# Optimization experiments

Hardware: AMD Instinct MI355X
Metric: run time of the kernel (lower is better)

## Reference

```python
import jax, jax.numpy as jnp
import numpy as np

HEADS = 12
HEAD_DIM = 64  # dim=768 // heads=12
NEG = -1e9


def setup_inputs() -> dict:
    key = jax.random.key(0)
    k1, k2, k3 = jax.random.split(key, 3)
    dim = HEADS * HEAD_DIM
    x = jax.random.normal(k1, (8, 1024, dim), dtype=jnp.float32)
    W_qkv = jax.random.normal(k2, (dim, 3 * dim), dtype=jnp.float32) * (dim ** -0.5)
    b_qkv = jnp.zeros((3 * dim,), dtype=jnp.float32)
    W_out = jax.random.normal(k3, (dim, dim), dtype=jnp.float32) * (dim ** -0.5)
    b_out = jnp.zeros((dim,), dtype=jnp.float32)
    return {"x": x, "W_qkv": W_qkv, "b_qkv": b_qkv, "W_out": W_out, "b_out": b_out}


def reference(x, W_qkv, b_qkv, W_out, b_out):
    B, T, C = x.shape
    qkv = x @ W_qkv + b_qkv                      # [B,T,3C]
    q, k, v = jnp.split(qkv, 3, axis=-1)
    # [B,T,C] -> [B,H,T,Dh]
    def split_heads(t):
        return t.reshape(B, T, HEADS, HEAD_DIM).transpose(0, 2, 1, 3)
    q, k, v = split_heads(q), split_heads(k), split_heads(v)
    att = jnp.einsum('bhqd,bhkd->bhqk', q, k) / jnp.sqrt(jnp.float32(HEAD_DIM))
    causal = jnp.tril(jnp.ones((T, T), dtype=bool))  # [T,T]
    att = jnp.where(causal[None, None], att, NEG)
    att = jax.nn.softmax(att, axis=-1)
    out = jnp.einsum('bhqk,bhkd->bhqd', att, v)  # [B,H,T,Dh]
    out = out.transpose(0, 2, 1, 3).reshape(B, T, C)
    return out @ W_out + b_out
```

## Files before the change

### kernel.cpp

```cpp
#include <hip/hip_runtime.h>
#include <hip/hip_bf16.h>

typedef unsigned short u16;
typedef unsigned int u32;
typedef __attribute__((ext_vector_type(8))) short short8;
typedef __attribute__((ext_vector_type(4))) float f32x4;
typedef __attribute__((ext_vector_type(16))) float f32x16;
typedef __attribute__((ext_vector_type(4))) unsigned int uint4v;

__device__ __forceinline__ u16 f2bf(float f) {
    union { float f; unsigned int u; } v; v.f = f;
    unsigned int u = v.u;
    return (u16)((u + 0x7FFFu + ((u >> 16) & 1u)) >> 16);
}
__device__ __forceinline__ u32 pk2(float a, float b) {
    return ((u32)f2bf(b) << 16) | (u32)f2bf(a);
}

__global__ void k_convert(const float* __restrict__ x, u16* __restrict__ o, int n4) {
    int i = blockIdx.x * blockDim.x + threadIdx.x;
    if (i < n4) {
        float4 v = ((const float4*)x)[i];
        ushort4 r;
        r.x = f2bf(v.x); r.y = f2bf(v.y); r.z = f2bf(v.z); r.w = f2bf(v.w);
        ((ushort4*)o)[i] = r;
    }
}

__global__ void k_transpose_bf(const float* __restrict__ W, u16* __restrict__ Wt, int K, int N) {
    __shared__ u16 t[32][33];
    int n0 = blockIdx.x * 32, k0 = blockIdx.y * 32;
    int tx = threadIdx.x, ty = threadIdx.y;
    #pragma unroll
    for (int i = 0; i < 4; i++) {
        t[ty + i * 8][tx] = f2bf(W[(long)(k0 + ty + i * 8) * N + n0 + tx]);
    }
    __syncthreads();
    #pragma unroll
    for (int i = 0; i < 4; i++) {
        Wt[(long)(n0 + ty + i * 8) * K + k0 + tx] = t[tx][ty + i * 8];
    }
}

__global__ void k_vt(const u16* __restrict__ qkv, u16* __restrict__ vt) {
    __shared__ u16 s[32][33];
    int t0 = blockIdx.x * 32, d0 = blockIdx.y * 32, bh = blockIdx.z;
    int b = bh / 12, h = bh - b * 12;
    int tx = threadIdx.x, ty = threadIdx.y;
    const u16* src = qkv + (size_t)(b * 1024 + t0) * 2304 + 1536 + h * 64 + d0;
    #pragma unroll
    for (int i = 0; i < 4; i++) {
        s[ty + i * 8][tx] = src[(size_t)(ty + i * 8) * 2304 + tx];
    }
    __syncthreads();
    u16* dst = vt + (size_t)bh * 65536 + (size_t)d0 * 1024 + t0;
    #pragma unroll
    for (int i = 0; i < 4; i++) {
        dst[(size_t)(ty + i * 8) * 1024 + tx] = s[tx][ty + i * 8];
    }
}

template<int EPI>
__global__ __launch_bounds__(256) void k_gemm_bt(
    const u16* __restrict__ A, const u16* __restrict__ Bt, const float* __restrict__ bias,
    float* __restrict__ Cf, u16* __restrict__ Cb,
    int M, int N, int K)
{
    __shared__ u16 lA[128][40];
    __shared__ u16 lB[128][40];
    int tid = threadIdx.x;
    int wid = tid >> 6, lane = tid & 63;
    int wm = wid >> 1, wn = wid & 1;
    int ln = lane & 15, gp = lane >> 4;
    int gm0 = blockIdx.x * 128, gn0 = blockIdx.y * 128;

    f32x4 zf = {0.f, 0.f, 0.f, 0.f};
    f32x4 acc[4][4];
    #pragma unroll
    for (int i = 0; i < 4; i++)
        #pragma unroll
        for (int j = 0; j < 4; j++) acc[i][j] = zf;

    int sr = tid >> 2;
    int sc = (tid & 3) * 8;

    for (int k0 = 0; k0 < K; k0 += 32) {
        #pragma unroll
        for (int j = 0; j < 2; j++) {
            int r = sr + j * 64;
            *(uint4v*)&lA[r][sc] = *(const uint4v*)&A[(long)(gm0 + r) * K + k0 + sc];
            *(uint4v*)&lB[r][sc] = *(const uint4v*)&Bt[(long)(gn0 + r) * K + k0 + sc];
        }
        __syncthreads();
        short8 af[4], bfr[4];
        #pragma unroll
        for (int i = 0; i < 4; i++) {
            af[i]  = *(const short8*)&lA[wm * 64 + i * 16 + ln][gp * 8];
            bfr[i] = *(const short8*)&lB[wn * 64 + i * 16 + ln][gp * 8];
        }
        #pragma unroll
        for (int i = 0; i < 4; i++)
            #pragma unroll
            for (int j = 0; j < 4; j++)
                acc[i][j] = __builtin_amdgcn_mfma_f32_16x16x32_bf16(af[i], bfr[j], acc[i][j], 0, 0, 0);
        __syncthreads();
    }

    #pragma unroll
    for (int i = 0; i < 4; i++) {
        #pragma unroll
        for (int j = 0; j < 4; j++) {
            #pragma unroll
            for (int r = 0; r < 4; r++) {
                int m = gm0 + wm * 64 + i * 16 + gp * 4 + r;
                int n = gn0 + wn * 64 + j * 16 + ln;
                float v = acc[i][j][r] + bias[n];
                if (EPI == 0) Cf[(long)m * N + n] = v;
                else          Cb[(long)m * N + n] = f2bf(v);
            }
        }
    }
}

__global__ __launch_bounds__(64, 3) void k_attn(
    const u16* __restrict__ qkv, const u16* __restrict__ Vt,
    u16* __restrict__ O)
{
    __shared__ u16 sK[2048];
    __shared__ u16 sV[2048];
    int lane = threadIdx.x;
    int l31 = lane & 31, hi = lane >> 5;
    int bx = blockIdx.x;
    int qtq = bx / 96, bh = bx - qtq * 96;
    int qt = 31 - qtq, q0 = qt * 32;
    int b = bh / 12, h = bh - b * 12;
    const u16* Qb  = qkv + (size_t)(b * 1024) * 2304 + h * 64;
    const u16* Kbb = Qb + 768;
    const u16* Vb  = Vt + (size_t)bh * 65536;

    short8 qf[4];
    #pragma unroll
    for (int ch = 0; ch < 4; ch++)
        qf[ch] = *(const short8*)&Qb[(size_t)(q0 + l31) * 2304 + ch * 16 + hi * 8];

    int rK = lane >> 3, cK = lane & 7;
    int rV = lane >> 2, cV = lane & 3;

    uint4v rk[4], rv[4];
    auto gload = [&](int kt) {
        #pragma unroll
        for (int j = 0; j < 4; j++) {
            int r = j * 8 + rK;
            rk[j] = *(const uint4v*)&Kbb[(size_t)(kt + r) * 2304 + cK * 8];
        }
        #pragma unroll
        for (int j = 0; j < 4; j++) {
            int r = j * 16 + rV;
            rv[j] = *(const uint4v*)&Vb[(size_t)r * 1024 + kt + cV * 8];
        }
    };
    auto swrite = [&]() {
        #pragma unroll
        for (int j = 0; j < 4; j++) {
            int r = j * 8 + rK;
            *(uint4v*)&sK[r * 64 + ((cK ^ (r & 7)) * 8)] = rk[j];
        }
        #pragma unroll
        for (int j = 0; j < 4; j++) {
            int r = j * 16 + rV;
            *(uint4v*)&sV[r * 32 + ((cV ^ (r & 3) ^ ((r >> 2) & 3)) * 8)] = rv[j];
        }
    };

    f32x16 o0 = {}, o1 = {};
    float mrun = -INFINITY, lsum = 0.f;
    const float SC = 0.18033688011f;
    int swl = l31 & 7;
    int swv = (l31 & 3) ^ ((l31 >> 2) & 3);

    int nit = qt + 1;
    gload(0);
    swrite();
    for (int it = 0; it < nit; it++) {
        int kt = it * 32;
        if (it + 1 < nit) gload(kt + 32);
        f32x16 sa = {}, sb = {};
        {
            short8 kf0 = *(const short8*)&sK[l31 * 64 + (((0 + hi) ^ swl) * 8)];
            short8 kf1 = *(const short8*)&sK[l31 * 64 + (((2 + hi) ^ swl) * 8)];
            short8 kf2 = *(const short8*)&sK[l31 * 64 + (((4 + hi) ^ swl) * 8)];
            short8 kf3 = *(const short8*)&sK[l31 * 64 + (((6 + hi) ^ swl) * 8)];
            sa = __builtin_amdgcn_mfma_f32_32x32x16_bf16(kf0, qf[0], sa, 0, 0, 0);
            sb = __builtin_amdgcn_mfma_f32_32x32x16_bf16(kf2, qf[2], sb, 0, 0, 0);
            sa = __builtin_amdgcn_mfma_f32_32x32x16_bf16(kf1, qf[1], sa, 0, 0, 0);
            sb = __builtin_amdgcn_mfma_f32_32x32x16_bf16(kf3, qf[3], sb, 0, 0, 0);
        }
        float raw[16];
        #pragma unroll
        for (int r = 0; r < 16; r++) raw[r] = sa[r] + sb[r];
        if (it == nit - 1) {
            #pragma unroll
            for (int r = 0; r < 16; r++) {
                int crow = (r & 3) + 8 * (r >> 2) + 4 * hi;
                raw[r] = (crow <= l31) ? raw[r] : -1e30f;
            }
        }
        float t8[8];
        #pragma unroll
        for (int i = 0; i < 8; i++) t8[i] = fmaxf(raw[i], raw[i + 8]);
        float t4a = fmaxf(t8[0], t8[1]), t4b = fmaxf(t8[2], t8[3]);
        float t4c = fmaxf(t8[4], t8[5]), t4d = fmaxf(t8[6], t8[7]);
        float tm = fmaxf(fmaxf(t4a, t4b), fmaxf(t4c, t4d));
        tm = fmaxf(tm, __shfl_xor(tm, 32));
        float stm = tm * SC;
        if (!__all(stm - mrun <= 8.0f)) {
            float mn = fmaxf(mrun, stm);
            float scale = exp2f(mrun - mn);
            lsum *= scale;
            #pragma unroll
            for (int r = 0; r < 16; r++) { o0[r] *= scale; o1[r] *= scale; }
            mrun = mn;
        }
        float ps[16];
        float rs = 0.f;
        #pragma unroll
        for (int r = 0; r < 16; r++) {
            ps[r] = exp2f(fmaf(raw[r], SC, -mrun));
            rs += ps[r];
        }
        rs += __shfl_xor(rs, 32);
        lsum += rs;
        u32 c[8], sw[8];
        #pragma unroll
        for (int i = 0; i < 8; i++) c[i] = pk2(ps[2 * i], ps[2 * i + 1]);
        #pragma unroll
        for (int i = 0; i < 8; i++) sw[i] = (u32)__shfl_xor((int)c[i], 32);
        union { u32 u[4]; short8 s8; } pb0, pb1;
        pb0.u[0] = hi ? sw[2] : c[0];
        pb0.u[1] = hi ? sw[3] : c[1];
        pb0.u[2] = hi ? c[2]  : sw[0];
        pb0.u[3] = hi ? c[3]  : sw[1];
        pb1.u[0] = hi ? sw[6] : c[4];
        pb1.u[1] = hi ? sw[7] : c[5];
        pb1.u[2] = hi ? c[6]  : sw[4];
        pb1.u[3] = hi ? c[7]  : sw[5];
        #pragma unroll
        for (int kh = 0; kh < 2; kh++) {
            const short8* pbp = kh ? &pb1.s8 : &pb0.s8;
            int p = (((kh * 2 + hi) ^ swv) * 8);
            short8 vf0 = *(const short8*)&sV[l31 * 32 + p];
            short8 vf1 = *(const short8*)&sV[(32 + l31) * 32 + p];
            o0 = __builtin_amdgcn_mfma_f32_32x32x16_bf16(vf0, *pbp, o0, 0, 0, 0);
            o1 = __builtin_amdgcn_mfma_f32_32x32x16_bf16(vf1, *pbp, o1, 0, 0, 0);
        }
        if (it + 1 < nit) swrite();
    }

    float inv = 1.0f / lsum;
    int t = q0 + l31;
    size_t base = ((size_t)(b * 1024 + t)) * 768 + h * 64;
    #pragma unroll
    for (int rq = 0; rq < 4; rq++) {
        ushort4 u0, u1;
        u0.x = f2bf(o0[4 * rq + 0] * inv); u0.y = f2bf(o0[4 * rq + 1] * inv);
        u0.z = f2bf(o0[4 * rq + 2] * inv); u0.w = f2bf(o0[4 * rq + 3] * inv);
        u1.x = f2bf(o1[4 * rq + 0] * inv); u1.y = f2bf(o1[4 * rq + 1] * inv);
        u1.z = f2bf(o1[4 * rq + 2] * inv); u1.w = f2bf(o1[4 * rq + 3] * inv);
        *(ushort4*)&O[base + rq * 8 + hi * 4]      = u0;
        *(ushort4*)&O[base + 32 + rq * 8 + hi * 4] = u1;
    }
}

extern "C" void kernel_launch(void* const* d_in, const int* in_sizes, int n_in,
                              void* d_out, int out_size, void* d_ws, size_t ws_size,
                              hipStream_t stream)
{
    const float* x     = (const float*)d_in[0];
    const float* W_qkv = (const float*)d_in[1];
    const float* b_qkv = (const float*)d_in[2];
    const float* W_out = (const float*)d_in[3];
    const float* b_out = (const float*)d_in[4];
    float* out = (float*)d_out;

    char* w = (char*)d_ws;
    u16* xb   = (u16*)w; w += (size_t)8192 * 768 * 2;
    u16* wqt  = (u16*)w; w += (size_t)2304 * 768 * 2;
    u16* wot  = (u16*)w; w += (size_t)768 * 768 * 2;
    u16* qkv  = (u16*)w; w += (size_t)8192 * 2304 * 2;
    u16* vt   = (u16*)w; w += (size_t)96 * 64 * 1024 * 2;
    u16* ao   = (u16*)w; w += (size_t)8192 * 768 * 2;

    k_convert<<<dim3(6144), 256, 0, stream>>>(x, xb, 1572864);
    k_transpose_bf<<<dim3(72, 24), dim3(32, 8), 0, stream>>>(W_qkv, wqt, 768, 2304);
    k_transpose_bf<<<dim3(24, 24), dim3(32, 8), 0, stream>>>(W_out, wot, 768, 768);
    k_gemm_bt<2><<<dim3(64, 18), 256, 0, stream>>>(xb, wqt, b_qkv, nullptr, qkv, 8192, 2304, 768);
    k_vt<<<dim3(32, 2, 96), dim3(32, 8), 0, stream>>>(qkv, vt);
    k_attn<<<dim3(3072), 64, 0, stream>>>(qkv, vt, ao);
    k_gemm_bt<0><<<dim3(64, 6), 256, 0, stream>>>(ao, wot, b_out, out, nullptr, 8192, 768, 768);
}
```

Before: 135.7 us.

## Triple-buffer GEMM tiles with direct global-to-LDS loads and swizzled layout

Rewrites the bf16 GEMM main loop to prefetch three K-slices ahead using global_load_lds, so global loads go straight into shared memory instead of passing through registers. Loads are overlapped with MFMA compute, with explicit vmcnt waits and barriers. The padded LDS layout is replaced by an XOR swizzle to avoid bank conflicts, and MFMA sections raise wave priority. This adds LDS footprint (three buffers) and relies on hand-managed waitcnt counts being correct.

```diff
diff --git a/kernel.cpp b/kernel.cpp
--- a/kernel.cpp
+++ b/kernel.cpp
@@ -8,6 +8,9 @@
 typedef __attribute__((ext_vector_type(16))) float f32x16;
 typedef __attribute__((ext_vector_type(4))) unsigned int uint4v;
 
+#define VMW(n) asm volatile("s_waitcnt vmcnt(" #n ")" ::: "memory")
+#define BARRIER() do { asm volatile("" ::: "memory"); __builtin_amdgcn_s_barrier(); asm volatile("" ::: "memory"); } while (0)
+
 __device__ __forceinline__ u16 f2bf(float f) {
     union { float f; unsigned int u; } v; v.f = f;
     unsigned int u = v.u;
@@ -15,6 +18,10 @@
 }
 __device__ __forceinline__ u32 pk2(float a, float b) {
     return ((u32)f2bf(b) << 16) | (u32)f2bf(a);
+}
+__device__ __forceinline__ void gload_lds16(const u16* g, u16* l) {
+    __builtin_amdgcn_global_load_lds((const __attribute__((address_space(1))) void*)g,
+                                     (__attribute__((address_space(3))) void*)l, 16, 0, 0);
 }
 
 __global__ void k_convert(const float* __restrict__ x, u16* __restrict__ o, int n4) {
@@ -66,8 +73,8 @@
     float* __restrict__ Cf, u16* __restrict__ Cb,
     int M, int N, int K)
 {
-    __shared__ u16 lA[128][40];
-    __shared__ u16 lB[128][40];
+    __shared__ u16 lA[3][128][32];
+    __shared__ u16 lB[3][128][32];
     int tid = threadIdx.x;
     int wid = tid >> 6, lane = tid & 63;
     int wm = wid >> 1, wn = wid & 1;
@@ -81,29 +88,57 @@
         #pragma unroll
         for (int j = 0; j < 4; j++) acc[i][j] = zf;
 
-    int sr = tid >> 2;
-    int sc = (tid & 3) * 8;
-
-    for (int k0 = 0; k0 < K; k0 += 32) {
-        #pragma unroll
-        for (int j = 0; j < 2; j++) {
-            int r = sr + j * 64;
-            *(uint4v*)&lA[r][sc] = *(const uint4v*)&A[(long)(gm0 + r) * K + k0 + sc];
-            *(uint4v*)&lB[r][sc] = *(const uint4v*)&Bt[(long)(gn0 + r) * K + k0 + sc];
-        }
-        __syncthreads();
+    int srow = wid * 32 + (lane >> 2);
+    int scol = (((lane & 3) ^ ((lane >> 3) & 3))) * 8;
+    const u16* gA0 = &A [(size_t)(gm0 + srow) * K + scol];
+    const u16* gA1 = gA0 + (size_t)16 * K;
+    const u16* gB0 = &Bt[(size_t)(gn0 + srow) * K + scol];
+    const u16* gB1 = gB0 + (size_t)16 * K;
+
+    int rc = (gp ^ ((ln >> 1) & 3)) * 8;
+
+    auto stage = [&](int k0, int bb) {
+        gload_lds16(gA0 + k0, &lA[bb][wid * 32][0]);
+        gload_lds16(gA1 + k0, &lA[bb][wid * 32 + 16][0]);
+        gload_lds16(gB0 + k0, &lB[bb][wid * 32][0]);
+        gload_lds16(gB1 + k0, &lB[bb][wid * 32 + 16][0]);
+    };
+    auto compute = [&](int bb) {
         short8 af[4], bfr[4];
         #pragma unroll
         for (int i = 0; i < 4; i++) {
-            af[i]  = *(const short8*)&lA[wm * 64 + i * 16 + ln][gp * 8];
-            bfr[i] = *(const short8*)&lB[wn * 64 + i * 16 + ln][gp * 8];
-        }
+            af[i]  = *(const short8*)&lA[bb][wm * 64 + i * 16 + ln][rc];
+            bfr[i] = *(const short8*)&lB[bb][wn * 64 + i * 16 + ln][rc];
+        }
+        __builtin_amdgcn_s_setprio(1);
         #pragma unroll
         for (int i = 0; i < 4; i++)
             #pragma unroll
             for (int j = 0; j < 4; j++)
                 acc[i][j] = __builtin_amdgcn_mfma_f32_16x16x32_bf16(af[i], bfr[j], acc[i][j], 0, 0, 0);
-        __syncthreads();
+        __builtin_amdgcn_s_setprio(0);
+    };
+
+    int nk = K >> 5;
+    stage(0, 0);
+    stage(32, 1);
+    stage(64, 2);
+    VMW(8);
+    BARRIER();
+    #pragma unroll 3
+    for (int t = 0; t < nk; ++t) {
+        int c = t % 3;
+        compute(c);
+        BARRIER();
+        if (t + 3 < nk) {
+            stage((t + 3) << 5, c);
+            VMW(8);
+        } else if (t + 2 < nk) {
+            VMW(4);
+        } else {
+            VMW(0);
+        }
+        BARRIER();
     }
 
     #pragma unroll
```

New measurement: 137.1 us. No clear change (+1.0%).
